# Performance work log

Measured on AMD Instinct MI355X. Metric: run time of the kernel, lower is better.

## Reference

```python
import jax, jax.numpy as jnp
import numpy as np

EPS = 1e-9
KERNEL = 3


def kernel_tile(x, kernel, stride):
    """im2col-style patch extraction. x: [B,H,W,...] -> [B,OH,OW,kernel*kernel,depth]."""
    B, H, W = x.shape[:3]
    depth = int(np.prod(x.shape[3:]))
    x = x.reshape(B, H, W, depth)
    OH = (H - kernel) // stride + 1
    OW = (W - kernel) // stride + 1
    patches = jnp.stack(
        [x[:, i:i + (OH - 1) * stride + 1:stride, j:j + (OW - 1) * stride + 1:stride, :]
         for i in range(kernel) for j in range(kernel)], axis=3)
    return patches  # [B,OH,OW,k*k,depth]


def em_routing(votes, i_act, beta_v, beta_a, routings):
    # votes: [B,S,S,I,O,16], i_act: [B,S,S,I], beta_*: [1,1,1,O]
    I, O = votes.shape[-3], votes.shape[-2]
    rr = jnp.full((I, O, 1), 1.0 / O, dtype=votes.dtype)
    i_act = i_act[..., None, None]           # [B,S,S,I,1,1]
    bv = beta_v[..., None, :, None]          # [1,1,1,1,O,1]
    ba = beta_a[..., None, :, None]
    it_min, it_max = 1.0, min(float(routings), 3.0)
    o_mean = o_act = None
    for it in range(routings):
        inv_temp = it_min + (it_max - it_min) * it / max(1.0, routings - 1.0)
        # M-step
        rr_prime = rr * i_act                                        # [B,S,S,I,O,1]
        rr_sum = jnp.sum(rr_prime, axis=-3, keepdims=True)           # [B,S,S,1,O,1]
        o_mean = jnp.sum(rr_prime * votes, axis=-3, keepdims=True) / rr_sum  # [B,S,S,1,O,16]
        o_stdv = jnp.sqrt(jnp.sum(rr_prime * jnp.square(votes - o_mean), axis=-3, keepdims=True) / rr_sum)
        o_cost = (bv + jnp.log(o_stdv + EPS)) * rr_sum               # [B,S,S,1,O,16]
        o_act = jax.nn.sigmoid(inv_temp * (ba - jnp.sum(o_cost, axis=-1, keepdims=True)))  # [B,S,S,1,O,1]
        if it < routings - 1:
            # E-step: log Gaussian prob of each vote under each output capsule
            o_p = (-jnp.sum(jnp.square(votes - o_mean) / (2.0 * jnp.square(o_stdv)), axis=-1, keepdims=True)
                   - jnp.sum(jnp.log(o_stdv + EPS), axis=-1, keepdims=True))  # [B,S,S,I,O,1]
            zz = jnp.log(o_act + EPS) + o_p
            rr = jax.nn.softmax(zz, axis=-2)                          # softmax over O
    pose = jnp.squeeze(o_mean, axis=-3)      # [B,S,S,O,16]
    act = jnp.squeeze(o_act, axis=(-3, -1))  # [B,S,S,O]
    return pose, act


def setup_inputs() -> dict:
    key = jax.random.key(0)
    ks = jax.random.split(key, 5)
    B, H, W, I_SIZE, O_SIZE = 4, 14, 14, 32, 32
    inputs_pose = jax.random.normal(ks[0], (B, H, W, I_SIZE, 4, 4), dtype=jnp.float32)
    inputs_activation = jax.random.uniform(ks[1], (B, H, W, I_SIZE), dtype=jnp.float32)
    w = jax.random.normal(ks[2], (1, 3 * 3 * I_SIZE, O_SIZE, 4, 4), dtype=jnp.float32)
    beta_v = 0.1 * jax.random.normal(ks[3], (1, 1, 1, O_SIZE), dtype=jnp.float32)
    beta_a = 0.1 * jax.random.normal(ks[4], (1, 1, 1, O_SIZE), dtype=jnp.float32)
    return {"inputs_pose": inputs_pose, "inputs_activation": inputs_activation,
            "w": w, "beta_v": beta_v, "beta_a": beta_a, "stride": 1, "routings": 3}


def reference(inputs_pose, inputs_activation, w, beta_v, beta_a, stride, routings):
    B = inputs_pose.shape[0]
    pose_size = inputs_pose.shape[-1]            # 4
    i_size = inputs_pose.shape[3]
    o_size = w.shape[2]
    tp = kernel_tile(inputs_pose, KERNEL, stride)        # [B,S,S,9,i*16]
    ta = kernel_tile(inputs_activation, KERNEL, stride)  # [B,S,S,9,i]
    S = ta.shape[1]
    I = KERNEL * KERNEL * i_size
    poses = tp.reshape(-1, I, pose_size, pose_size)      # [N,I,4,4], N = B*S*S
    acts = ta.reshape(B, S, S, I)
    # vote transform: per (input capsule, output capsule) 4x4 matmul
    votes = jnp.einsum('nipq,ioqr->niopr', poses, w[0])  # [N,I,O,4,4]
    votes = votes.reshape(B, S, S, I, o_size, pose_size * pose_size)
    pose, activation = em_routing(votes, acts, beta_v, beta_a, routings)
    pose = pose.reshape(B, S, S, o_size, pose_size, pose_size)
    return pose, activation
```

## Files before the change

kernel.cpp:

```cpp
#include <hip/hip_runtime.h>
#include <math.h>

namespace {

constexpr int SOUT = 12;
constexpr int OCAP = 32;
constexpr int PD   = 16;
constexpr int NI   = 288;
constexpr int SUBS = 4;
constexpr int ISUB = NI / SUBS;
constexpr int NPOS = 4 * SOUT * SOUT;
constexpr float EPSF = 1e-9f;
constexpr int CHUNK = 33 * 32;
constexpr int SSTR  = 36;
constexpr size_t POSE_OUT = (size_t)NPOS * OCAP * PD;

typedef float v2f __attribute__((ext_vector_type(2)));

__device__ __forceinline__ v2f vfma(v2f a, v2f b, v2f c) { return __builtin_elementwise_fma(a, b, c); }
__device__ __forceinline__ v2f splat(float a) { v2f r; r.x = a; r.y = a; return r; }

template<int CTRL>
__device__ __forceinline__ float dppf(float x) {
    return __int_as_float(__builtin_amdgcn_update_dpp(0, __float_as_int(x), CTRL, 0xF, 0xF, true));
}
#define SWZ16(x) __int_as_float(__builtin_amdgcn_ds_swizzle(__float_as_int(x), (16 << 10) | 0x1F))

__device__ __forceinline__ float redmax32(float x) {
    x = fmaxf(x, dppf<0xB1>(x));
    x = fmaxf(x, dppf<0x4E>(x));
    x = fmaxf(x, dppf<0x141>(x));
    x = fmaxf(x, dppf<0x140>(x));
    x = fmaxf(x, SWZ16(x));
    return x;
}
__device__ __forceinline__ float redsum32(float x) {
    x += dppf<0xB1>(x);
    x += dppf<0x4E>(x);
    x += dppf<0x141>(x);
    x += dppf<0x140>(x);
    x += SWZ16(x);
    return x;
}

__device__ __forceinline__ void loadW(const float* __restrict__ p, v2f (&W)[8]) {
    const float4 w0 = *reinterpret_cast<const float4*>(p);
    const float4 w1 = *reinterpret_cast<const float4*>(p + 4);
    const float4 w2 = *reinterpret_cast<const float4*>(p + 8);
    const float4 w3 = *reinterpret_cast<const float4*>(p + 12);
    W[0].x=w0.x; W[0].y=w0.y; W[1].x=w0.z; W[1].y=w0.w;
    W[2].x=w1.x; W[2].y=w1.y; W[3].x=w1.z; W[3].y=w1.w;
    W[4].x=w2.x; W[4].y=w2.y; W[5].x=w2.z; W[5].y=w2.w;
    W[6].x=w3.x; W[6].y=w3.y; W[7].x=w3.z; W[7].y=w3.w;
}

__device__ __forceinline__ void vote8(const float* __restrict__ pr, const v2f (&W)[8], v2f (&v)[8]) {
    #pragma unroll
    for (int p = 0; p < 4; ++p) {
        const float4 pv = *reinterpret_cast<const float4*>(pr + p * 4);
        #pragma unroll
        for (int h = 0; h < 2; ++h) {
            v2f acc = splat(pv.w) * W[6 + h];
            acc = vfma(splat(pv.z), W[4 + h], acc);
            acc = vfma(splat(pv.y), W[2 + h], acc);
            acc = vfma(splat(pv.x), W[0 + h], acc);
            v[p * 2 + h] = acc;
        }
    }
}

__device__ __forceinline__ constexpr int DH(int h) { return (h >> 1) * 4 + (h & 1) * 2; }

template<int SWEEP>
__global__ __launch_bounds__(256, 2)
void sweep_kernel(const float* __restrict__ pose_in,
                  const float* __restrict__ act_in,
                  const float* __restrict__ wmat,
                  const float* __restrict__ statbuf,
                  float* __restrict__ outbuf)
{
    __shared__ __align__(16) float sP[4 * ISUB * PD];
    __shared__ float sA[4 * ISUB];

    const int bid = blockIdx.x;
    const int yx  = bid >> 2;
    const int sub = bid & 3;
    const int y   = yx / SOUT;
    const int x   = yx % SOUT;

    const int t    = threadIdx.x;
    const int wave = t >> 6;
    const int lane = t & 63;
    const int o    = lane & 31;
    const int half = lane >> 5;

    {
        const float4* src = reinterpret_cast<const float4*>(pose_in);
        float4* dst = reinterpret_cast<float4*>(sP);
        for (int u = t; u < 4 * ISUB * 4; u += 256) {
            const int bs   = u / (ISUB * 4);
            const int r    = u - bs * (ISUB * 4);
            const int il   = r >> 2;
            const int comp = r & 3;
            const int ig   = sub * ISUB + il;
            const int k = ig >> 5, c = ig & 31;
            const int ki = k / 3, kj = k - ki * 3;
            const int cell = (bs * 14 + y + ki) * 14 + (x + kj);
            dst[u] = src[(size_t)(cell * 32 + c) * 4 + comp];
        }
        for (int u = t; u < 4 * ISUB; u += 256) {
            const int bs = u / ISUB;
            const int il = u - bs * ISUB;
            const int ig = sub * ISUB + il;
            const int k = ig >> 5, c = ig & 31;
            const int ki = k / 3, kj = k - ki * 3;
            const int cell = (bs * 14 + y + ki) * 14 + (x + kj);
            sA[u] = act_in[(size_t)cell * 32 + c];
        }
    }
    __syncthreads();

    const int n = wave * (SOUT * SOUT) + yx;

    float bias_r = 0.f;
    v2f i2r[8], ngr[8];
    if constexpr (SWEEP > 0) {
        const float* st = statbuf + ((size_t)n * OCAP + o) * SSTR;
        #pragma unroll
        for (int q = 0; q < 4; ++q) {
            const float4 a = *reinterpret_cast<const float4*>(st + q * 4);
            i2r[q*2].x = a.x; i2r[q*2].y = a.y; i2r[q*2+1].x = a.z; i2r[q*2+1].y = a.w;
            const float4 g = *reinterpret_cast<const float4*>(st + 16 + q * 4);
            ngr[q*2].x = g.x; ngr[q*2].y = g.y; ngr[q*2+1].x = g.z; ngr[q*2+1].y = g.w;
        }
        bias_r = st[32];
    }

    v2f s1[8], s2[8];
    float s0acc = 0.f;
    #pragma unroll
    for (int h = 0; h < 8; ++h) { s1[h] = splat(0.f); s2[h] = splat(0.f); }

    const float* wth = wmat + ((size_t)((sub * ISUB + half) * OCAP) + o) * PD;
    const float* pbase = sP + wave * ISUB * PD;
    const float* abase = sA + wave * ISUB;

    v2f WA[8], WB[8];
    loadW(wth, WA);

#define STEP(st_, Wc, Wn)                                                  \
    {                                                                      \
        if ((st_) < 35) loadW(wth + (size_t)((st_) + 1) * 1024, Wn);       \
        const int il = (st_) * 2 + half;                                   \
        v2f v[8];                                                          \
        vote8(pbase + il * PD, Wc, v);                                     \
        const float a_i = abase[il];                                       \
        float rrp;                                                         \
        if constexpr (SWEEP == 0) {                                        \
            rrp = a_i * (1.0f / 32.0f);                                    \
        } else {                                                           \
            v2f ts2 = splat(0.f);                                          \
            _Pragma("unroll")                                              \
            for (int h = 0; h < 8; ++h) {                                  \
                const v2f tmp = vfma(v[h], i2r[h], ngr[h]);                \
                ts2 = vfma(v[h], tmp, ts2);                                \
            }                                                              \
            const float zz = bias_r - (ts2.x + ts2.y);                     \
            const float m = redmax32(zz);                                  \
            const float e = __expf(zz - m);                                \
            const float es = redsum32(e);                                  \
            rrp = __fdividef(e, es) * a_i;                                 \
        }                                                                  \
        s0acc += rrp;                                                      \
        const v2f rr2 = splat(rrp);                                        \
        _Pragma("unroll")                                                  \
        for (int h = 0; h < 8; ++h) {                                      \
            const v2f rv = rr2 * v[h];                                     \
            s1[h] = s1[h] + rv;                                            \
            s2[h] = vfma(rv, v[h], s2[h]);                                 \
        }                                                                  \
    }

    #pragma unroll 1
    for (int kk = 0; kk < 18; ++kk) {
        STEP(2 * kk,     WA, WB);
        STEP(2 * kk + 1, WB, WA);
    }
#undef STEP

    #pragma unroll
    for (int h = 0; h < 8; ++h) {
        s1[h].x += __shfl_xor(s1[h].x, 32, 64);
        s1[h].y += __shfl_xor(s1[h].y, 32, 64);
        s2[h].x += __shfl_xor(s2[h].x, 32, 64);
        s2[h].y += __shfl_xor(s2[h].y, 32, 64);
    }
    s0acc += __shfl_xor(s0acc, 32, 64);

    if (half == 0) {
        float* dstc = outbuf + (size_t)(n * SUBS + sub) * CHUNK;
        #pragma unroll
        for (int h = 0; h < 8; ++h) {
            dstc[DH(h) * 32 + o]          = s1[h].x;
            dstc[(DH(h) + 1) * 32 + o]    = s1[h].y;
            dstc[(16 + DH(h)) * 32 + o]   = s2[h].x;
            dstc[(17 + DH(h)) * 32 + o]   = s2[h].y;
        }
        dstc[32 * 32 + o] = s0acc;
    }
}

template<int IT>
__global__ __launch_bounds__(256, 4)
void stats_kernel(const float* __restrict__ prev,
                  const float* __restrict__ beta_v,
                  const float* __restrict__ beta_a,
                  float* __restrict__ statbuf)
{
    const int n  = blockIdx.x;
    const int t  = threadIdx.x;
    const int oo = t >> 3, dp = t & 7, d0 = dp * 2;
    const float* base = prev + (size_t)n * (SUBS * CHUNK);
    float s0 = 0.f, S1a = 0.f, S1b = 0.f, S2a = 0.f, S2b = 0.f;
    #pragma unroll
    for (int s = 0; s < SUBS; ++s) {
        const float* c = base + s * CHUNK;
        s0  += c[32 * 32 + oo];
        S1a += c[(d0)      * 32 + oo];
        S1b += c[(d0 + 1)  * 32 + oo];
        S2a += c[(16 + d0) * 32 + oo];
        S2b += c[(17 + d0) * 32 + oo];
    }
    const float inv = 1.f / s0;
    const float m0 = S1a * inv, m1 = S1b * inv;
    const float v0 = fmaxf(fmaf(-m0, m0, S2a * inv), 0.f);
    const float v1 = fmaxf(fmaf(-m1, m1, S2b * inv), 0.f);
    const float i20 = 0.5f / fmaxf(v0, 1e-30f);
    const float i21 = 0.5f / fmaxf(v1, 1e-30f);
    float ll = __logf(sqrtf(v0) + EPSF) + __logf(sqrtf(v1) + EPSF);
    float c0 = m0 * m0 * i20 + m1 * m1 * i21;

    float* st = statbuf + ((size_t)n * OCAP + oo) * SSTR;
    st[d0]          = i20;
    st[d0 + 1]      = i21;
    st[16 + d0]     = -2.f * m0 * i20;
    st[17 + d0]     = -2.f * m1 * i21;

    #pragma unroll
    for (int m = 1; m <= 4; m <<= 1) {
        ll += __shfl_xor(ll, m, 8);
        c0 += __shfl_xor(c0, m, 8);
    }
    if (dp == 0) {
        const float cost = s0 * fmaf(16.f, beta_v[oo], ll);
        const float oact = 1.f / (1.f + __expf(-(float)IT * (beta_a[oo] - cost)));
        st[32] = __logf(oact + EPSF) - ll - c0;
    }
}

__global__ __launch_bounds__(256, 4)
void final_kernel(const float* __restrict__ prev,
                  const float* __restrict__ beta_v,
                  const float* __restrict__ beta_a,
                  float* __restrict__ out)
{
    const int n  = blockIdx.x;
    const int t  = threadIdx.x;
    const int oo = t >> 3, dp = t & 7, d0 = dp * 2;
    const float* base = prev + (size_t)n * (SUBS * CHUNK);
    float s0 = 0.f, S1a = 0.f, S1b = 0.f, S2a = 0.f, S2b = 0.f;
    #pragma unroll
    for (int s = 0; s < SUBS; ++s) {
        const float* c = base + s * CHUNK;
        s0  += c[32 * 32 + oo];
        S1a += c[(d0)      * 32 + oo];
        S1b += c[(d0 + 1)  * 32 + oo];
        S2a += c[(16 + d0) * 32 + oo];
        S2b += c[(17 + d0) * 32 + oo];
    }
    const float inv = 1.f / s0;
    const float m0 = S1a * inv, m1 = S1b * inv;
    out[(size_t)n * (OCAP * PD) + oo * PD + d0]     = m0;
    out[(size_t)n * (OCAP * PD) + oo * PD + d0 + 1] = m1;

    const float v0 = fmaxf(fmaf(-m0, m0, S2a * inv), 0.f);
    const float v1 = fmaxf(fmaf(-m1, m1, S2b * inv), 0.f);
    float lt = __logf(sqrtf(v0) + EPSF) + __logf(sqrtf(v1) + EPSF);
    lt += __shfl_xor(lt, 1, 8);
    lt += __shfl_xor(lt, 2, 8);
    lt += __shfl_xor(lt, 4, 8);
    if (dp == 0) {
        const float cost = s0 * fmaf(16.f, beta_v[oo], lt);
        const float oact = 1.f / (1.f + __expf(-3.0f * (beta_a[oo] - cost)));
        out[POSE_OUT + (size_t)n * OCAP + oo] = oact;
    }
}

}

extern "C" void kernel_launch(void* const* d_in, const int* in_sizes, int n_in,
                              void* d_out, int out_size, void* d_ws, size_t ws_size,
                              hipStream_t stream) {
    const float* pose_in = (const float*)d_in[0];
    const float* act_in  = (const float*)d_in[1];
    const float* wmat    = (const float*)d_in[2];
    const float* beta_v  = (const float*)d_in[3];
    const float* beta_a  = (const float*)d_in[4];
    float* out = (float*)d_out;

    float* bufA    = (float*)d_ws;
    float* bufB    = bufA + (size_t)NPOS * SUBS * CHUNK;
    float* statbuf = bufB + (size_t)NPOS * SUBS * CHUNK;

    dim3 block(256);
    dim3 gridS(NPOS);
    dim3 gridN(NPOS);

    sweep_kernel<0><<<gridS, block, 0, stream>>>(pose_in, act_in, wmat, nullptr, bufA);
    stats_kernel<1><<<gridN, block, 0, stream>>>(bufA, beta_v, beta_a, statbuf);
    sweep_kernel<1><<<gridS, block, 0, stream>>>(pose_in, act_in, wmat, statbuf, bufB);
    stats_kernel<2><<<gridN, block, 0, stream>>>(bufB, beta_v, beta_a, statbuf);
    sweep_kernel<2><<<gridS, block, 0, stream>>>(pose_in, act_in, wmat, statbuf, bufA);
    final_kernel<<<gridN, block, 0, stream>>>(bufA, beta_v, beta_a, out);
}
```

Baseline: 126.2 us.

## Split pose columns across wave halves instead of input capsules in sweep kernel

The sweep kernel now has each 32-lane half-wave compute two of the four pose columns for every input capsule, rather than alternating input capsules between halves. The per-capsule exponent term is combined across halves with a cross-lane shuffle, which removes the end-of-kernel half-wave reduction and halves the per-lane accumulator and stat register footprint. Weight loads become 8-byte loads of four capsules at a time, replacing the explicit double-buffered prefetch. The partial-sum layout changes to per-output-capsule rows with stride 34 so writes and stats reads are contiguous, and the stats load moves before the barrier. The trade-off is an extra shuffle per capsule in the routing sweeps and smaller, less coalesced weight loads.

```diff
diff --git a/kernel.cpp b/kernel.cpp
--- a/kernel.cpp
+++ b/kernel.cpp
@@ -11,7 +11,7 @@
 constexpr int ISUB = NI / SUBS;
 constexpr int NPOS = 4 * SOUT * SOUT;
 constexpr float EPSF = 1e-9f;
-constexpr int CHUNK = 33 * 32;
+constexpr int CHUNK = 34 * 32;
 constexpr int SSTR  = 36;
 constexpr size_t POSE_OUT = (size_t)NPOS * OCAP * PD;
 
@@ -42,34 +42,6 @@
     x += SWZ16(x);
     return x;
 }
-
-__device__ __forceinline__ void loadW(const float* __restrict__ p, v2f (&W)[8]) {
-    const float4 w0 = *reinterpret_cast<const float4*>(p);
-    const float4 w1 = *reinterpret_cast<const float4*>(p + 4);
-    const float4 w2 = *reinterpret_cast<const float4*>(p + 8);
-    const float4 w3 = *reinterpret_cast<const float4*>(p + 12);
-    W[0].x=w0.x; W[0].y=w0.y; W[1].x=w0.z; W[1].y=w0.w;
-    W[2].x=w1.x; W[2].y=w1.y; W[3].x=w1.z; W[3].y=w1.w;
-    W[4].x=w2.x; W[4].y=w2.y; W[5].x=w2.z; W[5].y=w2.w;
-    W[6].x=w3.x; W[6].y=w3.y; W[7].x=w3.z; W[7].y=w3.w;
-}
-
-__device__ __forceinline__ void vote8(const float* __restrict__ pr, const v2f (&W)[8], v2f (&v)[8]) {
-    #pragma unroll
-    for (int p = 0; p < 4; ++p) {
-        const float4 pv = *reinterpret_cast<const float4*>(pr + p * 4);
-        #pragma unroll
-        for (int h = 0; h < 2; ++h) {
-            v2f acc = splat(pv.w) * W[6 + h];
-            acc = vfma(splat(pv.z), W[4 + h], acc);
-            acc = vfma(splat(pv.y), W[2 + h], acc);
-            acc = vfma(splat(pv.x), W[0 + h], acc);
-            v[p * 2 + h] = acc;
-        }
-    }
-}
-
-__device__ __forceinline__ constexpr int DH(int h) { return (h >> 1) * 4 + (h & 1) * 2; }
 
 template<int SWEEP>
 __global__ __launch_bounds__(256, 2)
@@ -92,7 +64,7 @@
     const int wave = t >> 6;
     const int lane = t & 63;
     const int o    = lane & 31;
-    const int half = lane >> 5;
+    const int rh   = lane >> 5;
 
     {
         const float4* src = reinterpret_cast<const float4*>(pose_in);
@@ -118,96 +90,101 @@
             sA[u] = act_in[(size_t)cell * 32 + c];
         }
     }
-    __syncthreads();
 
     const int n = wave * (SOUT * SOUT) + yx;
 
     float bias_r = 0.f;
-    v2f i2r[8], ngr[8];
+    v2f i2r[4], ngr[4];
     if constexpr (SWEEP > 0) {
         const float* st = statbuf + ((size_t)n * OCAP + o) * SSTR;
         #pragma unroll
-        for (int q = 0; q < 4; ++q) {
-            const float4 a = *reinterpret_cast<const float4*>(st + q * 4);
-            i2r[q*2].x = a.x; i2r[q*2].y = a.y; i2r[q*2+1].x = a.z; i2r[q*2+1].y = a.w;
-            const float4 g = *reinterpret_cast<const float4*>(st + 16 + q * 4);
-            ngr[q*2].x = g.x; ngr[q*2].y = g.y; ngr[q*2+1].x = g.z; ngr[q*2+1].y = g.w;
+        for (int p = 0; p < 4; ++p) {
+            i2r[p] = *reinterpret_cast<const v2f*>(st + p * 4 + 2 * rh);
+            ngr[p] = *reinterpret_cast<const v2f*>(st + 16 + p * 4 + 2 * rh);
         }
         bias_r = st[32];
     }
-
-    v2f s1[8], s2[8];
+    __syncthreads();
+
+    v2f s1[4], s2[4];
     float s0acc = 0.f;
     #pragma unroll
-    for (int h = 0; h < 8; ++h) { s1[h] = splat(0.f); s2[h] = splat(0.f); }
-
-    const float* wth = wmat + ((size_t)((sub * ISUB + half) * OCAP) + o) * PD;
-    const float* pbase = sP + wave * ISUB * PD;
-    const float* abase = sA + wave * ISUB;
-
-    v2f WA[8], WB[8];
-    loadW(wth, WA);
-
-#define STEP(st_, Wc, Wn)                                                  \
-    {                                                                      \
-        if ((st_) < 35) loadW(wth + (size_t)((st_) + 1) * 1024, Wn);       \
-        const int il = (st_) * 2 + half;                                   \
-        v2f v[8];                                                          \
-        vote8(pbase + il * PD, Wc, v);                                     \
-        const float a_i = abase[il];                                       \
-        float rrp;                                                         \
-        if constexpr (SWEEP == 0) {                                        \
-            rrp = a_i * (1.0f / 32.0f);                                    \
-        } else {                                                           \
-            v2f ts2 = splat(0.f);                                          \
-            _Pragma("unroll")                                              \
-            for (int h = 0; h < 8; ++h) {                                  \
-                const v2f tmp = vfma(v[h], i2r[h], ngr[h]);                \
-                ts2 = vfma(v[h], tmp, ts2);                                \
-            }                                                              \
-            const float zz = bias_r - (ts2.x + ts2.y);                     \
-            const float m = redmax32(zz);                                  \
-            const float e = __expf(zz - m);                                \
-            const float es = redsum32(e);                                  \
-            rrp = __fdividef(e, es) * a_i;                                 \
-        }                                                                  \
-        s0acc += rrp;                                                      \
-        const v2f rr2 = splat(rrp);                                        \
-        _Pragma("unroll")                                                  \
-        for (int h = 0; h < 8; ++h) {                                      \
-            const v2f rv = rr2 * v[h];                                     \
-            s1[h] = s1[h] + rv;                                            \
-            s2[h] = vfma(rv, v[h], s2[h]);                                 \
-        }                                                                  \
-    }
+    for (int p = 0; p < 4; ++p) { s1[p] = splat(0.f); s2[p] = splat(0.f); }
+
+    const float* wl = wmat + ((size_t)(sub * ISUB) * OCAP + o) * PD + rh * 2;
+    const float* pb = sP + wave * ISUB * PD;
+    const float* ab = sA + wave * ISUB;
 
     #pragma unroll 1
-    for (int kk = 0; kk < 18; ++kk) {
-        STEP(2 * kk,     WA, WB);
-        STEP(2 * kk + 1, WB, WA);
-    }
-#undef STEP
-
-    #pragma unroll
-    for (int h = 0; h < 8; ++h) {
-        s1[h].x += __shfl_xor(s1[h].x, 32, 64);
-        s1[h].y += __shfl_xor(s1[h].y, 32, 64);
-        s2[h].x += __shfl_xor(s2[h].x, 32, 64);
-        s2[h].y += __shfl_xor(s2[h].y, 32, 64);
-    }
-    s0acc += __shfl_xor(s0acc, 32, 64);
-
-    if (half == 0) {
-        float* dstc = outbuf + (size_t)(n * SUBS + sub) * CHUNK;
+    for (int it = 0; it < ISUB / 4; ++it) {
+        const int i0 = it * 4;
+
+        v2f W[4][4];
+        float av[4];
         #pragma unroll
-        for (int h = 0; h < 8; ++h) {
-            dstc[DH(h) * 32 + o]          = s1[h].x;
-            dstc[(DH(h) + 1) * 32 + o]    = s1[h].y;
-            dstc[(16 + DH(h)) * 32 + o]   = s2[h].x;
-            dstc[(17 + DH(h)) * 32 + o]   = s2[h].y;
-        }
-        dstc[32 * 32 + o] = s0acc;
-    }
+        for (int ii = 0; ii < 4; ++ii) {
+            const float* wi = wl + (size_t)(i0 + ii) * 512;
+            #pragma unroll
+            for (int q = 0; q < 4; ++q)
+                W[ii][q] = *reinterpret_cast<const v2f*>(wi + q * 4);
+            av[ii] = ab[i0 + ii];
+        }
+
+        #pragma unroll
+        for (int ii = 0; ii < 4; ++ii) {
+            const float* pr = pb + (i0 + ii) * PD;
+            const float4 p0 = *reinterpret_cast<const float4*>(pr);
+            const float4 p1 = *reinterpret_cast<const float4*>(pr + 4);
+            const float4 p2 = *reinterpret_cast<const float4*>(pr + 8);
+            const float4 p3 = *reinterpret_cast<const float4*>(pr + 12);
+
+            v2f v[4];
+            v[0] = vfma(splat(p0.x), W[ii][0], vfma(splat(p0.y), W[ii][1],
+                   vfma(splat(p0.z), W[ii][2], splat(p0.w) * W[ii][3])));
+            v[1] = vfma(splat(p1.x), W[ii][0], vfma(splat(p1.y), W[ii][1],
+                   vfma(splat(p1.z), W[ii][2], splat(p1.w) * W[ii][3])));
+            v[2] = vfma(splat(p2.x), W[ii][0], vfma(splat(p2.y), W[ii][1],
+                   vfma(splat(p2.z), W[ii][2], splat(p2.w) * W[ii][3])));
+            v[3] = vfma(splat(p3.x), W[ii][0], vfma(splat(p3.y), W[ii][1],
+                   vfma(splat(p3.z), W[ii][2], splat(p3.w) * W[ii][3])));
+
+            float rrp;
+            if constexpr (SWEEP == 0) {
+                rrp = av[ii] * (1.0f / 32.0f);
+            } else {
+                v2f ts2 = splat(0.f);
+                #pragma unroll
+                for (int p = 0; p < 4; ++p) {
+                    const v2f tmp = vfma(v[p], i2r[p], ngr[p]);
+                    ts2 = vfma(v[p], tmp, ts2);
+                }
+                float ts = ts2.x + ts2.y;
+                ts += __shfl_xor(ts, 32, 64);
+                const float zz = bias_r - ts;
+                const float m = redmax32(zz);
+                const float e = __expf(zz - m);
+                const float es = redsum32(e);
+                rrp = __fdividef(e, es) * av[ii];
+            }
+
+            s0acc += rrp;
+            const v2f rr2 = splat(rrp);
+            #pragma unroll
+            for (int p = 0; p < 4; ++p) {
+                const v2f rv = rr2 * v[p];
+                s1[p] = s1[p] + rv;
+                s2[p] = vfma(rv, v[p], s2[p]);
+            }
+        }
+    }
+
+    float* dstc = outbuf + (size_t)(n * SUBS + sub) * CHUNK + o * 34;
+    #pragma unroll
+    for (int p = 0; p < 4; ++p) {
+        *reinterpret_cast<float2*>(dstc + p * 4 + 2 * rh)      = float2{s1[p].x, s1[p].y};
+        *reinterpret_cast<float2*>(dstc + 16 + p * 4 + 2 * rh) = float2{s2[p].x, s2[p].y};
+    }
+    if (rh == 0) dstc[32] = s0acc;
 }
 
 template<int IT>
@@ -220,16 +197,16 @@
     const int n  = blockIdx.x;
     const int t  = threadIdx.x;
     const int oo = t >> 3, dp = t & 7, d0 = dp * 2;
-    const float* base = prev + (size_t)n * (SUBS * CHUNK);
+    const float* base = prev + (size_t)n * (SUBS * CHUNK) + oo * 34;
     float s0 = 0.f, S1a = 0.f, S1b = 0.f, S2a = 0.f, S2b = 0.f;
     #pragma unroll
     for (int s = 0; s < SUBS; ++s) {
         const float* c = base + s * CHUNK;
-        s0  += c[32 * 32 + oo];
-        S1a += c[(d0)      * 32 + oo];
-        S1b += c[(d0 + 1)  * 32 + oo];
-        S2a += c[(16 + d0) * 32 + oo];
-        S2b += c[(17 + d0) * 32 + oo];
+        s0  += c[32];
+        S1a += c[d0];
+        S1b += c[d0 + 1];
+        S2a += c[16 + d0];
+        S2b += c[17 + d0];
     }
     const float inv = 1.f / s0;
     const float m0 = S1a * inv, m1 = S1b * inv;
@@ -267,16 +244,16 @@
     const int n  = blockIdx.x;
     const int t  = threadIdx.x;
     const int oo = t >> 3, dp = t & 7, d0 = dp * 2;
-    const float* base = prev + (size_t)n * (SUBS * CHUNK);
+    const float* base = prev + (size_t)n * (SUBS * CHUNK) + oo * 34;
     float s0 = 0.f, S1a = 0.f, S1b = 0.f, S2a = 0.f, S2b = 0.f;
     #pragma unroll
     for (int s = 0; s < SUBS; ++s) {
         const float* c = base + s * CHUNK;
-        s0  += c[32 * 32 + oo];
-        S1a += c[(d0)      * 32 + oo];
-        S1b += c[(d0 + 1)  * 32 + oo];
-        S2a += c[(16 + d0) * 32 + oo];
-        S2b += c[(17 + d0) * 32 + oo];
+        s0  += c[32];
+        S1a += c[d0];
+        S1b += c[d0 + 1];
+        S2a += c[16 + d0];
+        S2b += c[17 + d0];
     }
     const float inv = 1.f / s0;
     const float m0 = S1a * inv, m1 = S1b * inv;
@@ -313,7 +290,7 @@
     float* statbuf = bufB + (size_t)NPOS * SUBS * CHUNK;
 
     dim3 block(256);
-    dim3 gridS(NPOS);
+    dim3 gridS(144 * SUBS);
     dim3 gridN(NPOS);
 
     sweep_kernel<0><<<gridS, block, 0, stream>>>(pose_in, act_in, wmat, nullptr, bufA);
```

Measured after the change: 191.6 us. 1.52x slower.

## Fuse routing statistics into sweep kernel and drop softmax max reduction

Applied to the files above, without the earlier changes.

Removes the separate stats kernels. Each sweep block now reduces the previous partial sums itself and computes mean, variance, log terms and the activation bias in registers. The two halves of a wave exchange their per-dimension stats with cross-lane shuffles, and the partial-sum layout index is changed to match. The softmax no longer subtracts the max before exponentiating, and launch bounds are raised to allow more resident blocks. This saves two launches and a stats buffer round trip, at the cost of redundant stat computation in every sub-block and a risk of exp overflow without the max shift.

```diff
diff --git a/kernel.cpp b/kernel.cpp
--- a/kernel.cpp
+++ b/kernel.cpp
@@ -12,7 +12,6 @@
 constexpr int NPOS = 4 * SOUT * SOUT;
 constexpr float EPSF = 1e-9f;
 constexpr int CHUNK = 33 * 32;
-constexpr int SSTR  = 36;
 constexpr size_t POSE_OUT = (size_t)NPOS * OCAP * PD;
 
 typedef float v2f __attribute__((ext_vector_type(2)));
@@ -26,14 +25,6 @@
 }
 #define SWZ16(x) __int_as_float(__builtin_amdgcn_ds_swizzle(__float_as_int(x), (16 << 10) | 0x1F))
 
-__device__ __forceinline__ float redmax32(float x) {
-    x = fmaxf(x, dppf<0xB1>(x));
-    x = fmaxf(x, dppf<0x4E>(x));
-    x = fmaxf(x, dppf<0x141>(x));
-    x = fmaxf(x, dppf<0x140>(x));
-    x = fmaxf(x, SWZ16(x));
-    return x;
-}
 __device__ __forceinline__ float redsum32(float x) {
     x += dppf<0xB1>(x);
     x += dppf<0x4E>(x);
@@ -69,14 +60,16 @@
     }
 }
 
-__device__ __forceinline__ constexpr int DH(int h) { return (h >> 1) * 4 + (h & 1) * 2; }
+__device__ __forceinline__ constexpr int DH(int h) { return 2 * h; }
 
 template<int SWEEP>
-__global__ __launch_bounds__(256, 2)
+__global__ __launch_bounds__(256, 5)
 void sweep_kernel(const float* __restrict__ pose_in,
                   const float* __restrict__ act_in,
                   const float* __restrict__ wmat,
-                  const float* __restrict__ statbuf,
+                  const float* __restrict__ beta_v,
+                  const float* __restrict__ beta_a,
+                  const float* __restrict__ prev,
                   float* __restrict__ outbuf)
 {
     __shared__ __align__(16) float sP[4 * ISUB * PD];
@@ -118,23 +111,63 @@
             sA[u] = act_in[(size_t)cell * 32 + c];
         }
     }
-    __syncthreads();
 
     const int n = wave * (SOUT * SOUT) + yx;
 
     float bias_r = 0.f;
     v2f i2r[8], ngr[8];
     if constexpr (SWEEP > 0) {
-        const float* st = statbuf + ((size_t)n * OCAP + o) * SSTR;
-        #pragma unroll
-        for (int q = 0; q < 4; ++q) {
-            const float4 a = *reinterpret_cast<const float4*>(st + q * 4);
-            i2r[q*2].x = a.x; i2r[q*2].y = a.y; i2r[q*2+1].x = a.z; i2r[q*2+1].y = a.w;
-            const float4 g = *reinterpret_cast<const float4*>(st + 16 + q * 4);
-            ngr[q*2].x = g.x; ngr[q*2].y = g.y; ngr[q*2+1].x = g.z; ngr[q*2+1].y = g.w;
-        }
-        bias_r = st[32];
-    }
+        const float* base = prev + (size_t)n * (SUBS * CHUNK);
+        float S0 = 0.f, S1[8], S2[8];
+        #pragma unroll
+        for (int d = 0; d < 8; ++d) { S1[d] = 0.f; S2[d] = 0.f; }
+        #pragma unroll
+        for (int s = 0; s < SUBS; ++s) {
+            const float* c = base + s * CHUNK;
+            S0 += c[32 * 32 + o];
+            #pragma unroll
+            for (int d = 0; d < 8; ++d) {
+                S1[d] += c[(half * 8 + d) * 32 + o];
+                S2[d] += c[(16 + half * 8 + d) * 32 + o];
+            }
+        }
+        const float inv = 1.f / S0;
+        float ll = 0.f, c0 = 0.f;
+        v2f i2own[4], ngown[4];
+        #pragma unroll
+        for (int m = 0; m < 4; ++m) {
+            const float m0 = S1[2*m] * inv, m1 = S1[2*m+1] * inv;
+            const float v0 = fmaxf(fmaf(-m0, m0, S2[2*m]   * inv), 0.f);
+            const float v1 = fmaxf(fmaf(-m1, m1, S2[2*m+1] * inv), 0.f);
+            const float i20 = 0.5f / fmaxf(v0, 1e-30f);
+            const float i21 = 0.5f / fmaxf(v1, 1e-30f);
+            ll += __logf(sqrtf(v0) + EPSF) + __logf(sqrtf(v1) + EPSF);
+            c0 += m0 * m0 * i20 + m1 * m1 * i21;
+            i2own[m].x = i20;            i2own[m].y = i21;
+            ngown[m].x = -2.f * m0 * i20; ngown[m].y = -2.f * m1 * i21;
+        }
+        ll += __shfl_xor(ll, 32, 64);
+        c0 += __shfl_xor(c0, 32, 64);
+        const float cost = S0 * fmaf(16.f, beta_v[o], ll);
+        const float oact = 1.f / (1.f + __expf(-(float)SWEEP * (beta_a[o] - cost)));
+        bias_r = __logf(oact + EPSF) - ll - c0;
+        #pragma unroll
+        for (int m = 0; m < 4; ++m) {
+            v2f oi2, ong;
+            oi2.x = __shfl_xor(i2own[m].x, 32, 64);
+            oi2.y = __shfl_xor(i2own[m].y, 32, 64);
+            ong.x = __shfl_xor(ngown[m].x, 32, 64);
+            ong.y = __shfl_xor(ngown[m].y, 32, 64);
+            if (half == 0) {
+                i2r[m] = i2own[m]; i2r[4+m] = oi2;
+                ngr[m] = ngown[m]; ngr[4+m] = ong;
+            } else {
+                i2r[m] = oi2; i2r[4+m] = i2own[m];
+                ngr[m] = ong; ngr[4+m] = ngown[m];
+            }
+        }
+    }
+    __syncthreads();
 
     v2f s1[8], s2[8];
     float s0acc = 0.f;
@@ -165,9 +198,9 @@
                 const v2f tmp = vfma(v[h], i2r[h], ngr[h]);                \
                 ts2 = vfma(v[h], tmp, ts2);                                \
             }                                                              \
+             \
             const float zz = bias_r - (ts2.x + ts2.y);                     \
-            const float m = redmax32(zz);                                  \
-            const float e = __expf(zz - m);                                \
+            const float e = __expf(zz);                                    \
             const float es = redsum32(e);                                  \
             rrp = __fdividef(e, es) * a_i;                                 \
         }                                                                  \
@@ -207,54 +240,6 @@
             dstc[(17 + DH(h)) * 32 + o]   = s2[h].y;
         }
         dstc[32 * 32 + o] = s0acc;
-    }
-}
-
-template<int IT>
-__global__ __launch_bounds__(256, 4)
-void stats_kernel(const float* __restrict__ prev,
-                  const float* __restrict__ beta_v,
-                  const float* __restrict__ beta_a,
-                  float* __restrict__ statbuf)
-{
-    const int n  = blockIdx.x;
-    const int t  = threadIdx.x;
-    const int oo = t >> 3, dp = t & 7, d0 = dp * 2;
-    const float* base = prev + (size_t)n * (SUBS * CHUNK);
-    float s0 = 0.f, S1a = 0.f, S1b = 0.f, S2a = 0.f, S2b = 0.f;
-    #pragma unroll
-    for (int s = 0; s < SUBS; ++s) {
-        const float* c = base + s * CHUNK;
-        s0  += c[32 * 32 + oo];
-        S1a += c[(d0)      * 32 + oo];
-        S1b += c[(d0 + 1)  * 32 + oo];
-        S2a += c[(16 + d0) * 32 + oo];
-        S2b += c[(17 + d0) * 32 + oo];
-    }
-    const float inv = 1.f / s0;
-    const float m0 = S1a * inv, m1 = S1b * inv;
-    const float v0 = fmaxf(fmaf(-m0, m0, S2a * inv), 0.f);
-    const float v1 = fmaxf(fmaf(-m1, m1, S2b * inv), 0.f);
-    const float i20 = 0.5f / fmaxf(v0, 1e-30f);
-    const float i21 = 0.5f / fmaxf(v1, 1e-30f);
-    float ll = __logf(sqrtf(v0) + EPSF) + __logf(sqrtf(v1) + EPSF);
-    float c0 = m0 * m0 * i20 + m1 * m1 * i21;
-
-    float* st = statbuf + ((size_t)n * OCAP + oo) * SSTR;
-    st[d0]          = i20;
-    st[d0 + 1]      = i21;
-    st[16 + d0]     = -2.f * m0 * i20;
-    st[17 + d0]     = -2.f * m1 * i21;
-
-    #pragma unroll
-    for (int m = 1; m <= 4; m <<= 1) {
-        ll += __shfl_xor(ll, m, 8);
-        c0 += __shfl_xor(c0, m, 8);
-    }
-    if (dp == 0) {
-        const float cost = s0 * fmaf(16.f, beta_v[oo], ll);
-        const float oact = 1.f / (1.f + __expf(-(float)IT * (beta_a[oo] - cost)));
-        st[32] = __logf(oact + EPSF) - ll - c0;
     }
 }
 
@@ -308,18 +293,15 @@
     const float* beta_a  = (const float*)d_in[4];
     float* out = (float*)d_out;
 
-    float* bufA    = (float*)d_ws;
-    float* bufB    = bufA + (size_t)NPOS * SUBS * CHUNK;
-    float* statbuf = bufB + (size_t)NPOS * SUBS * CHUNK;
+    float* bufA = (float*)d_ws;
+    float* bufB = bufA + (size_t)NPOS * SUBS * CHUNK;
 
     dim3 block(256);
-    dim3 gridS(NPOS);
-    dim3 gridN(NPOS);
-
-    sweep_kernel<0><<<gridS, block, 0, stream>>>(pose_in, act_in, wmat, nullptr, bufA);
-    stats_kernel<1><<<gridN, block, 0, stream>>>(bufA, beta_v, beta_a, statbuf);
-    sweep_kernel<1><<<gridS, block, 0, stream>>>(pose_in, act_in, wmat, statbuf, bufB);
-    stats_kernel<2><<<gridN, block, 0, stream>>>(bufB, beta_v, beta_a, statbuf);
-    sweep_kernel<2><<<gridS, block, 0, stream>>>(pose_in, act_in, wmat, statbuf, bufA);
-    final_kernel<<<gridN, block, 0, stream>>>(bufA, beta_v, beta_a, out);
-}
+    dim3 gridS(144 * SUBS);
+    dim3 gridF(NPOS);
+
+    sweep_kernel<0><<<gridS, block, 0, stream>>>(pose_in, act_in, wmat, beta_v, beta_a, nullptr, bufA);
+    sweep_kernel<1><<<gridS, block, 0, stream>>>(pose_in, act_in, wmat, beta_v, beta_a, bufA, bufB);
+    sweep_kernel<2><<<gridS, block, 0, stream>>>(pose_in, act_in, wmat, beta_v, beta_a, bufB, bufA);
+    final_kernel<<<gridF, block, 0, stream>>>(bufA, beta_v, beta_a, out);
+}
```

After: 313.3 us. +148.2%, slower.
